# Kernel optimization log

Hardware: AMD Instinct MI355X
Metric: run time of the kernel (lower is better)

The kernel has to match this reference:

```python
import jax, jax.numpy as jnp
import numpy as np

H = 64   # hidden_dim
E = 5    # num_edge_features
F = 6    # num_node_features
B, W, N = 8, 12, 200
LN_EPS = 1e-5


def _lstm_layer(x, Wih, Whh, bih, bhh):
    # x: [BN, W, Fin] -> full output sequence [BN, W, H] (PyTorch gate order i,f,g,o)
    BN = x.shape[0]
    h0 = jnp.zeros((BN, Whh.shape[1]), x.dtype)
    def step(carry, xt):
        h, c = carry
        g = xt @ Wih.T + h @ Whh.T + (bih + bhh)
        i, f, gg, o = jnp.split(g, 4, axis=-1)
        c = jax.nn.sigmoid(f) * c + jax.nn.sigmoid(i) * jnp.tanh(gg)
        h = jax.nn.sigmoid(o) * jnp.tanh(c)
        return (h, c), h
    _, ys = jax.lax.scan(step, (h0, h0), jnp.swapaxes(x, 0, 1))
    return jnp.swapaxes(ys, 0, 1)


def _layernorm(x, g, b):
    mu = jnp.mean(x, axis=-1, keepdims=True)
    var = jnp.mean(jnp.square(x - mu), axis=-1, keepdims=True)
    return (x - mu) * jax.lax.rsqrt(var + LN_EPS) * g + b


def setup_inputs() -> dict:
    key = jax.random.key(0)
    ks = jax.random.split(key, 32)
    s = 0.05
    d = {
        'node_features': jax.random.normal(ks[0], (B, W, N, F), jnp.float32),
        'edge_features': jax.random.normal(ks[1], (B, W, N, N, E), jnp.float32),
        'adjacency': jax.random.uniform(ks[2], (B, N, N), jnp.float32),
        # LSTM layer 0 (input F) and layer 1 (input H)
        'Wih0': jax.random.normal(ks[3], (4 * H, F), jnp.float32) * s,
        'Whh0': jax.random.normal(ks[4], (4 * H, H), jnp.float32) * s,
        'bih0': jax.random.normal(ks[5], (4 * H,), jnp.float32) * s,
        'bhh0': jax.random.normal(ks[6], (4 * H,), jnp.float32) * s,
        'Wih1': jax.random.normal(ks[7], (4 * H, H), jnp.float32) * s,
        'Whh1': jax.random.normal(ks[8], (4 * H, H), jnp.float32) * s,
        'bih1': jax.random.normal(ks[9], (4 * H,), jnp.float32) * s,
        'bhh1': jax.random.normal(ks[10], (4 * H,), jnp.float32) * s,
        # 2 GCN layers: linear, edge projection, layernorm
        'gcn_W': jax.random.normal(ks[11], (2, H, H), jnp.float32) * s,
        'gcn_b': jax.random.normal(ks[12], (2, H), jnp.float32) * s,
        'ep_W': jax.random.normal(ks[13], (2, H, E), jnp.float32) * s,
        'ep_b': jax.random.normal(ks[14], (2, H), jnp.float32) * s,
        'ln_g': jnp.ones((2, H), jnp.float32),
        'ln_b': jnp.zeros((2, H), jnp.float32),
        # edge MLP: (2H+E) -> H -> H//2 -> 1
        'mlp_W1': jax.random.normal(ks[15], (H, 2 * H + E), jnp.float32) * s,
        'mlp_b1': jax.random.normal(ks[16], (H,), jnp.float32) * s,
        'mlp_W2': jax.random.normal(ks[17], (H // 2, H), jnp.float32) * s,
        'mlp_b2': jax.random.normal(ks[18], (H // 2,), jnp.float32) * s,
        'mlp_W3': jax.random.normal(ks[19], (1, H // 2), jnp.float32) * s,
        'mlp_b3': jax.random.normal(ks[20], (1,), jnp.float32) * s,
    }
    return d


def reference(node_features, edge_features, adjacency,
              Wih0, Whh0, bih0, bhh0, Wih1, Whh1, bih1, bhh1,
              gcn_W, gcn_b, ep_W, ep_b, ln_g, ln_b,
              mlp_W1, mlp_b1, mlp_W2, mlp_b2, mlp_W3, mlp_b3):
    Bn, Wn, Nn, _ = node_features.shape
    # [B,W,N,F] -> [B*N, W, F]
    x = jnp.transpose(node_features, (0, 2, 1, 3)).reshape(Bn * Nn, Wn, -1)
    y0 = _lstm_layer(x, Wih0, Whh0, bih0, bhh0)      # dropout between layers: eval mode (identity)
    y1 = _lstm_layer(y0, Wih1, Whh1, bih1, bhh1)
    h = y1[:, -1, :].reshape(Bn, Nn, H)

    edge_last = edge_features[:, -1]                 # [B,N,N,E]
    for i in range(2):
        edge_h = edge_last @ ep_W[i].T + ep_b[i]     # [B,N,N,H]
        messages = jnp.einsum('bij,bijn->bin', adjacency, edge_h)
        updated = h @ gcn_W[i].T + gcn_b[i] + messages
        h = jax.nn.relu(_layernorm(updated, ln_g[i], ln_b[i]))
        # dropout: eval mode (identity)

    h_i = jnp.broadcast_to(h[:, :, None, :], (Bn, Nn, Nn, H))
    h_j = jnp.broadcast_to(h[:, None, :, :], (Bn, Nn, Nn, H))
    edge_input = jnp.concatenate([h_i, h_j, edge_last], axis=-1)  # [B,N,N,2H+E]
    z = jax.nn.relu(edge_input @ mlp_W1.T + mlp_b1)
    z = jax.nn.relu(z @ mlp_W2.T + mlp_b2)
    logits = (z @ mlp_W3.T + mlp_b3)[..., 0]
    return jax.nn.sigmoid(logits)
```

## Files before the change

### kernel.cpp

```cpp
#include <hip/hip_runtime.h>
#include <math.h>


#define Hd   64
#define Ed   5
#define Fd   6
#define Bd   8
#define Wd   12
#define Nd   200
#define NSEQ (Bd*Nd)
#define NG   (4*Hd)
#define NEDGE (Bd*Nd*Nd)
#define LNEPS 1e-5f

__device__ __forceinline__ float sigm(float x) { return 1.0f / (1.0f + __expf(-x)); }
__device__ __forceinline__ float tanh_fast(float x) {
  float ax = fabsf(x);
  float t  = __expf(-2.0f * ax);
  float r  = (1.0f - t) / (1.0f + t);
  return copysignf(r, x);
}

__global__ __launch_bounds__(256) void k_prep(const float* __restrict__ Wih1,
                                              float* __restrict__ Wt1) {
  int k = blockIdx.x;
  int j = threadIdx.x;
  Wt1[k * NG + j] = Wih1[j * Hd + k];
}

__global__ __launch_bounds__(256) void k_lstm0(
    const float* __restrict__ nf,
    const float* __restrict__ Wih0, const float* __restrict__ Whh0,
    const float* __restrict__ bih0, const float* __restrict__ bhh0,
    float* __restrict__ y0)
{
  __shared__ float x_sh[Wd * Fd];
  __shared__ float h_sh[Hd];
  __shared__ float gate_sh[NG];

  const int tid = threadIdx.x;
  const int seq = blockIdx.x;
  const int b = seq / Nd, n = seq % Nd;

  if (tid < Wd * Fd) {
    int t = tid / Fd, f = tid % Fd;
    x_sh[tid] = nf[((b * Wd + t) * Nd + n) * Fd + f];
  }
  if (tid < Hd) h_sh[tid] = 0.f;

  const int j = tid;
  float4 wh[16];
  const float4* wrow = (const float4*)(Whh0 + j * Hd);
  #pragma unroll
  for (int q = 0; q < 16; ++q) wh[q] = wrow[q];
  float wx[Fd];
  #pragma unroll
  for (int f = 0; f < Fd; ++f) wx[f] = Wih0[j * Fd + f];
  const float bias = bih0[j] + bhh0[j];
  const int jt = j >> 6;

  float c = 0.f;
  __syncthreads();

  for (int t = 0; t < Wd; ++t) {
    const float* xp = x_sh + t * Fd;
    float a0 = bias, a1 = 0.f, a2 = 0.f, a3 = 0.f;
    #pragma unroll
    for (int f = 0; f < Fd; ++f) a1 += xp[f] * wx[f];
    const float4* h4 = (const float4*)h_sh;
    #pragma unroll
    for (int q = 0; q < 16; ++q) {
      float4 hv = h4[q];
      float d = hv.x * wh[q].x + hv.y * wh[q].y + hv.z * wh[q].z + hv.w * wh[q].w;
      if ((q & 3) == 0) a0 += d; else if ((q & 3) == 1) a1 += d;
      else if ((q & 3) == 2) a2 += d; else a3 += d;
    }
    float acc = (a0 + a1) + (a2 + a3);
    gate_sh[j] = (jt == 2) ? tanh_fast(acc) : sigm(acc);
    __syncthreads();
    if (tid < Hd) {
      float iv = gate_sh[tid];
      float fv = gate_sh[64 + tid];
      float gv = gate_sh[128 + tid];
      float ov = gate_sh[192 + tid];
      c = fv * c + iv * gv;
      float h = ov * tanh_fast(c);
      h_sh[tid] = h;
      y0[seq * (Wd * Hd) + t * Hd + tid] = h;
    }
    __syncthreads();
  }
}

__global__ __launch_bounds__(256) void k_xproj1(
    const float* __restrict__ y0,
    const float* __restrict__ Wt1,
    const float* __restrict__ bih1, const float* __restrict__ bhh1,
    float* __restrict__ G1)
{
  __shared__ float ysh[64 * 65];
  __shared__ float osh[2 * 64 * 65];

  const int tid  = threadIdx.x;
  const int row0 = blockIdx.x * 64;
  for (int idx = tid; idx < 64 * 64; idx += 256) {
    int r = idx >> 6, k = idx & 63;
    ysh[r * 65 + k] = y0[(row0 + r) * Hd + k];
  }
  __syncthreads();

  const int w = __builtin_amdgcn_readfirstlane(tid >> 6);
  const int r = tid & 63;
  float acc[64];
  #pragma unroll
  for (int c = 0; c < 64; ++c) acc[c] = 0.f;

  const float* wbase = Wt1 + (w << 6);
  #pragma unroll 2
  for (int k = 0; k < 64; ++k) {
    float yv = ysh[r * 65 + k];
    const float* wk = wbase + k * NG;
    #pragma unroll
    for (int c = 0; c < 64; ++c) acc[c] = fmaf(yv, wk[c], acc[c]);
  }
  #pragma unroll
  for (int c = 0; c < 64; ++c) acc[c] += bih1[(w << 6) + c] + bhh1[(w << 6) + c];

  #pragma unroll
  for (int p = 0; p < 2; ++p) {
    __syncthreads();
    if ((w >> 1) == p) {
      float* orow = osh + ((w & 1) * 64 + r) * 65;
      #pragma unroll
      for (int c = 0; c < 64; ++c) orow[c] = acc[c];
    }
    __syncthreads();
    for (int idx = tid; idx < 2 * 64 * 64; idx += 256) {
      int c  = idx & 127;
      int rr = idx >> 7;
      G1[(row0 + rr) * NG + p * 128 + c] =
          osh[((c >> 6) * 64 + rr) * 65 + (c & 63)];
    }
  }
}

__global__ __launch_bounds__(256) void k_lstm1(
    const float* __restrict__ G1,
    const float* __restrict__ Whh1,
    float* __restrict__ hout)
{
  __shared__ float h_sh[Hd];
  __shared__ float gate_sh[NG];

  const int tid = threadIdx.x;
  const int seq = blockIdx.x;
  if (tid < Hd) h_sh[tid] = 0.f;

  const int j = tid;
  float4 wh[16];
  const float4* wrow = (const float4*)(Whh1 + j * Hd);
  #pragma unroll
  for (int q = 0; q < 16; ++q) wh[q] = wrow[q];
  const int jt = j >> 6;
  float c = 0.f;

  float g_cur = G1[(seq * Wd + 0) * NG + j];
  __syncthreads();

  for (int t = 0; t < Wd; ++t) {
    float g_next = (t + 1 < Wd) ? G1[(seq * Wd + t + 1) * NG + j] : 0.f;
    float a0 = g_cur;
    float a1 = 0.f, a2 = 0.f, a3 = 0.f;
    const float4* h4 = (const float4*)h_sh;
    #pragma unroll
    for (int q = 0; q < 16; ++q) {
      float4 hv = h4[q];
      float d = hv.x * wh[q].x + hv.y * wh[q].y + hv.z * wh[q].z + hv.w * wh[q].w;
      if ((q & 3) == 0) a0 += d; else if ((q & 3) == 1) a1 += d;
      else if ((q & 3) == 2) a2 += d; else a3 += d;
    }
    float acc = (a0 + a1) + (a2 + a3);
    gate_sh[j] = (jt == 2) ? tanh_fast(acc) : sigm(acc);
    __syncthreads();
    if (tid < Hd) {
      float iv = gate_sh[tid];
      float fv = gate_sh[64 + tid];
      float gv = gate_sh[128 + tid];
      float ov = gate_sh[192 + tid];
      c = fv * c + iv * gv;
      float h = ov * tanh_fast(c);
      h_sh[tid] = h;
      if (t == Wd - 1) hout[seq * Hd + tid] = h;
    }
    __syncthreads();
    g_cur = g_next;
  }
}

__global__ __launch_bounds__(256) void k_wsum(
    const float* __restrict__ ef, const float* __restrict__ adj,
    float* __restrict__ wsum)
{
  const int row = blockIdx.x;
  const int b = row / Nd, i = row % Nd;
  const int tid = threadIdx.x;
  float p[6] = {0.f, 0.f, 0.f, 0.f, 0.f, 0.f};
  if (tid < Nd) {
    float a = adj[(b * Nd + i) * Nd + tid];
    const float* e = ef + (((b * Wd + (Wd - 1)) * Nd + i) * Nd + tid) * Ed;
    p[5] = a;
    #pragma unroll
    for (int k = 0; k < Ed; ++k) p[k] = a * e[k];
  }
  #pragma unroll
  for (int k = 0; k < 6; ++k) {
    float v = p[k];
    for (int off = 32; off > 0; off >>= 1) v += __shfl_down(v, off);
    p[k] = v;
  }
  __shared__ float red[4][6];
  if ((tid & 63) == 0) {
    #pragma unroll
    for (int k = 0; k < 6; ++k) red[tid >> 6][k] = p[k];
  }
  __syncthreads();
  if (tid < 6)
    wsum[row * 6 + tid] = red[0][tid] + red[1][tid] + red[2][tid] + red[3][tid];
}

__global__ __launch_bounds__(256) void k_gcn(
    const float* __restrict__ hin, const float* __restrict__ wsum,
    const float* __restrict__ gcn_W, const float* __restrict__ gcn_b,
    const float* __restrict__ ep_W,  const float* __restrict__ ep_b,
    const float* __restrict__ ln_g,  const float* __restrict__ ln_b,
    int round, float* __restrict__ hout)
{
  const int row = blockIdx.x * 4 + (threadIdx.x >> 6);
  const int u   = threadIdx.x & 63;
  const float* gw = gcn_W + (round * Hd + u) * Hd;
  const float* ew = ep_W  + (round * Hd + u) * Ed;
  const float* hr = hin + row * Hd;
  const float* wsr = wsum + row * 6;

  float acc = gcn_b[round * Hd + u] + wsr[5] * ep_b[round * Hd + u];
  #pragma unroll
  for (int e = 0; e < Ed; ++e) acc += wsr[e] * ew[e];
  #pragma unroll 8
  for (int k = 0; k < Hd; ++k) acc += hr[k] * gw[k];

  float mu = acc;
  #pragma unroll
  for (int off = 1; off < 64; off <<= 1) mu += __shfl_xor(mu, off);
  mu *= (1.f / 64.f);
  float d = acc - mu;
  float var = d * d;
  #pragma unroll
  for (int off = 1; off < 64; off <<= 1) var += __shfl_xor(var, off);
  var *= (1.f / 64.f);
  float v = d * rsqrtf(var + LNEPS) * ln_g[round * Hd + u] + ln_b[round * Hd + u];
  hout[row * Hd + u] = fmaxf(v, 0.f);
}

__global__ __launch_bounds__(128) void k_uv(
    const float* __restrict__ h, const float* __restrict__ W1,
    const float* __restrict__ b1,
    float* __restrict__ u, float* __restrict__ vt)
{
  const int row = blockIdx.x;
  const int tid = threadIdx.x;
  const float* hr = h + row * Hd;
  if (tid < 64) {
    const float* wr = W1 + tid * 133;
    float acc = b1[tid];
    #pragma unroll 8
    for (int k = 0; k < Hd; ++k) acc += hr[k] * wr[k];
    u[row * Hd + tid] = acc;
  } else {
    const int n = tid - 64;
    const float* wr = W1 + n * 133 + 64;
    float acc = 0.f;
    #pragma unroll 8
    for (int k = 0; k < Hd; ++k) acc += hr[k] * wr[k];
    vt[n * NSEQ + row] = acc;
  }
}

__global__ __launch_bounds__(256) void k_mlp(
    const float* __restrict__ ef,
    const float* __restrict__ u, const float* __restrict__ vt,
    const float* __restrict__ W1,
    const float* __restrict__ W2, const float* __restrict__ b2,
    const float* __restrict__ W3, const float* __restrict__ b3,
    float* __restrict__ out)
{
  const int idx = blockIdx.x * 256 + threadIdx.x;
  const int b   = idx / (Nd * Nd);
  const int rem = idx - b * Nd * Nd;
  const int i   = rem / Nd;
  const int jj  = rem - i * Nd;

  const float* e = ef + (((b * Wd + (Wd - 1)) * Nd + i) * Nd + jj) * Ed;
  float e5[Ed];
  #pragma unroll
  for (int q = 0; q < Ed; ++q) e5[q] = e[q];

  const float* ur = u + (b * Nd + i) * Hd;
  const int vcol = b * Nd + jj;

  float z1[64];
  #pragma unroll
  for (int k = 0; k < 64; ++k) {
    float acc = ur[k] + vt[k * NSEQ + vcol];
    const float* w1c = W1 + k * 133 + 128;
    #pragma unroll
    for (int q = 0; q < Ed; ++q) acc += e5[q] * w1c[q];
    z1[k] = fmaxf(acc, 0.f);
  }

  float logit = b3[0];
  #pragma unroll 4
  for (int o = 0; o < 32; ++o) {
    float a0 = b2[o], a1 = 0.f, a2 = 0.f, a3 = 0.f;
    const float* w2 = W2 + o * 64;
    #pragma unroll
    for (int k = 0; k < 64; k += 4) {
      a0 += w2[k]     * z1[k];
      a1 += w2[k + 1] * z1[k + 1];
      a2 += w2[k + 2] * z1[k + 2];
      a3 += w2[k + 3] * z1[k + 3];
    }
    float z2 = fmaxf((a0 + a1) + (a2 + a3), 0.f);
    logit += W3[o] * z2;
  }
  out[idx] = 1.f / (1.f + __expf(-logit));
}

extern "C" void kernel_launch(void* const* d_in, const int* in_sizes, int n_in,
                              void* d_out, int out_size, void* d_ws, size_t ws_size,
                              hipStream_t stream) {
  (void)in_sizes; (void)n_in; (void)out_size; (void)ws_size;
  const float* nf   = (const float*)d_in[0];
  const float* ef   = (const float*)d_in[1];
  const float* adj  = (const float*)d_in[2];
  const float* Wih0 = (const float*)d_in[3];
  const float* Whh0 = (const float*)d_in[4];
  const float* bih0 = (const float*)d_in[5];
  const float* bhh0 = (const float*)d_in[6];
  const float* Wih1 = (const float*)d_in[7];
  const float* Whh1 = (const float*)d_in[8];
  const float* bih1 = (const float*)d_in[9];
  const float* bhh1 = (const float*)d_in[10];
  const float* gcnW = (const float*)d_in[11];
  const float* gcnB = (const float*)d_in[12];
  const float* epW  = (const float*)d_in[13];
  const float* epB  = (const float*)d_in[14];
  const float* lnG  = (const float*)d_in[15];
  const float* lnB  = (const float*)d_in[16];
  const float* W1   = (const float*)d_in[17];
  const float* b1   = (const float*)d_in[18];
  const float* W2   = (const float*)d_in[19];
  const float* b2   = (const float*)d_in[20];
  const float* W3   = (const float*)d_in[21];
  const float* b3   = (const float*)d_in[22];
  float* out = (float*)d_out;

  float* ws  = (float*)d_ws;
  float* y0  = ws;
  float* G1  = y0  + 1228800;
  float* Wt1 = G1  + 4915200;
  float* h0  = Wt1 + 16384;
  float* wsm = h0  + 102400;
  float* hA  = wsm + 9600;
  float* hB  = hA  + 102400;
  float* uu  = hB  + 102400;
  float* vt  = uu  + 102400;

  k_prep  <<<64,   256, 0, stream>>>(Wih1, Wt1);
  k_lstm0 <<<NSEQ, 256, 0, stream>>>(nf, Wih0, Whh0, bih0, bhh0, y0);
  k_xproj1<<<300,  256, 0, stream>>>(y0, Wt1, bih1, bhh1, G1);
  k_lstm1 <<<NSEQ, 256, 0, stream>>>(G1, Whh1, h0);
  k_wsum  <<<1600, 256, 0, stream>>>(ef, adj, wsm);
  k_gcn   <<<400,  256, 0, stream>>>(h0, wsm, gcnW, gcnB, epW, epB, lnG, lnB, 0, hA);
  k_gcn   <<<400,  256, 0, stream>>>(hA, wsm, gcnW, gcnB, epW, epB, lnG, lnB, 1, hB);
  k_uv    <<<1600, 128, 0, stream>>>(hB, W1, b1, uu, vt);
  k_mlp   <<<1250, 256, 0, stream>>>(ef, uu, vt, W1, W2, b2, W3, b3, out);
}
```

Measured before the change: 277.2 us.

## Compute all LSTM gates per thread in one wave and fuse node-stage kernels

Both LSTM kernels now run one 64-thread wavefront per sequence. Each thread keeps all four gate rows of the recurrent weights in registers and computes i, f, g, o and the cell update itself. This removes the shared gate buffer and one block barrier per timestep, at the cost of about four times the serial FMA work per thread and much higher register pressure. The adjacency/edge weighted-sum, both GCN rounds and the u/v projection are merged into one per-row kernel. That removes three launches and the intermediate global buffers, though most threads in that fused kernel sit idle during the GCN and projection phases.

```diff
diff --git a/kernel.cpp b/kernel.cpp
--- a/kernel.cpp
+++ b/kernel.cpp
@@ -28,7 +28,7 @@
   Wt1[k * NG + j] = Wih1[j * Hd + k];
 }
 
-__global__ __launch_bounds__(256) void k_lstm0(
+__global__ __launch_bounds__(64, 1) void k_lstm0(
     const float* __restrict__ nf,
     const float* __restrict__ Wih0, const float* __restrict__ Whh0,
     const float* __restrict__ bih0, const float* __restrict__ bhh0,
@@ -36,59 +36,66 @@
 {
   __shared__ float x_sh[Wd * Fd];
   __shared__ float h_sh[Hd];
-  __shared__ float gate_sh[NG];
-
-  const int tid = threadIdx.x;
+
+  const int u   = threadIdx.x;
   const int seq = blockIdx.x;
   const int b = seq / Nd, n = seq % Nd;
 
-  if (tid < Wd * Fd) {
-    int t = tid / Fd, f = tid % Fd;
-    x_sh[tid] = nf[((b * Wd + t) * Nd + n) * Fd + f];
-  }
-  if (tid < Hd) h_sh[tid] = 0.f;
-
-  const int j = tid;
-  float4 wh[16];
-  const float4* wrow = (const float4*)(Whh0 + j * Hd);
-  #pragma unroll
-  for (int q = 0; q < 16; ++q) wh[q] = wrow[q];
-  float wx[Fd];
-  #pragma unroll
-  for (int f = 0; f < Fd; ++f) wx[f] = Wih0[j * Fd + f];
-  const float bias = bih0[j] + bhh0[j];
-  const int jt = j >> 6;
+  for (int idx = u; idx < Wd * Fd; idx += 64) {
+    int t = idx / Fd, f = idx % Fd;
+    x_sh[idx] = nf[((b * Wd + t) * Nd + n) * Fd + f];
+  }
+  h_sh[u] = 0.f;
+
+  float4 wh[4][16];
+  #pragma unroll
+  for (int g = 0; g < 4; ++g) {
+    const float4* wrow = (const float4*)(Whh0 + (g * 64 + u) * Hd);
+    #pragma unroll
+    for (int q = 0; q < 16; ++q) wh[g][q] = wrow[q];
+  }
+  float wx[4][Fd];
+  #pragma unroll
+  for (int g = 0; g < 4; ++g)
+    #pragma unroll
+    for (int f = 0; f < Fd; ++f) wx[g][f] = Wih0[(g * 64 + u) * Fd + f];
+  float bias[4];
+  #pragma unroll
+  for (int g = 0; g < 4; ++g) bias[g] = bih0[g * 64 + u] + bhh0[g * 64 + u];
 
   float c = 0.f;
   __syncthreads();
 
   for (int t = 0; t < Wd; ++t) {
-    const float* xp = x_sh + t * Fd;
-    float a0 = bias, a1 = 0.f, a2 = 0.f, a3 = 0.f;
-    #pragma unroll
-    for (int f = 0; f < Fd; ++f) a1 += xp[f] * wx[f];
+    float xv[Fd];
+    #pragma unroll
+    for (int f = 0; f < Fd; ++f) xv[f] = x_sh[t * Fd + f];
+    float4 hv[16];
     const float4* h4 = (const float4*)h_sh;
     #pragma unroll
-    for (int q = 0; q < 16; ++q) {
-      float4 hv = h4[q];
-      float d = hv.x * wh[q].x + hv.y * wh[q].y + hv.z * wh[q].z + hv.w * wh[q].w;
-      if ((q & 3) == 0) a0 += d; else if ((q & 3) == 1) a1 += d;
-      else if ((q & 3) == 2) a2 += d; else a3 += d;
-    }
-    float acc = (a0 + a1) + (a2 + a3);
-    gate_sh[j] = (jt == 2) ? tanh_fast(acc) : sigm(acc);
-    __syncthreads();
-    if (tid < Hd) {
-      float iv = gate_sh[tid];
-      float fv = gate_sh[64 + tid];
-      float gv = gate_sh[128 + tid];
-      float ov = gate_sh[192 + tid];
-      c = fv * c + iv * gv;
-      float h = ov * tanh_fast(c);
-      h_sh[tid] = h;
-      y0[seq * (Wd * Hd) + t * Hd + tid] = h;
-    }
-    __syncthreads();
+    for (int q = 0; q < 16; ++q) hv[q] = h4[q];
+
+    float g4[4];
+    #pragma unroll
+    for (int g = 0; g < 4; ++g) {
+      float a0 = bias[g], a1 = 0.f, a2 = 0.f, a3 = 0.f;
+      #pragma unroll
+      for (int f = 0; f < Fd; ++f) a1 += xv[f] * wx[g][f];
+      #pragma unroll
+      for (int q = 0; q < 16; ++q) {
+        float d = hv[q].x * wh[g][q].x + hv[q].y * wh[g][q].y +
+                  hv[q].z * wh[g][q].z + hv[q].w * wh[g][q].w;
+        if ((q & 3) == 0) a0 += d; else if ((q & 3) == 1) a1 += d;
+        else if ((q & 3) == 2) a2 += d; else a3 += d;
+      }
+      float acc = (a0 + a1) + (a2 + a3);
+      g4[g] = (g == 2) ? tanh_fast(acc) : sigm(acc);
+    }
+    c = g4[1] * c + g4[0] * g4[2];
+    float h = g4[3] * tanh_fast(c);
+    h_sh[u] = h;
+    __syncthreads();
+    y0[seq * (Wd * Hd) + t * Hd + u] = h;
   }
 }
 
@@ -144,66 +151,84 @@
   }
 }
 
-__global__ __launch_bounds__(256) void k_lstm1(
+__global__ __launch_bounds__(64, 1) void k_lstm1(
     const float* __restrict__ G1,
     const float* __restrict__ Whh1,
     float* __restrict__ hout)
 {
   __shared__ float h_sh[Hd];
-  __shared__ float gate_sh[NG];
-
-  const int tid = threadIdx.x;
+
+  const int u   = threadIdx.x;
   const int seq = blockIdx.x;
-  if (tid < Hd) h_sh[tid] = 0.f;
-
-  const int j = tid;
-  float4 wh[16];
-  const float4* wrow = (const float4*)(Whh1 + j * Hd);
-  #pragma unroll
-  for (int q = 0; q < 16; ++q) wh[q] = wrow[q];
-  const int jt = j >> 6;
+  h_sh[u] = 0.f;
+
+  float4 wh[4][16];
+  #pragma unroll
+  for (int g = 0; g < 4; ++g) {
+    const float4* wrow = (const float4*)(Whh1 + (g * 64 + u) * Hd);
+    #pragma unroll
+    for (int q = 0; q < 16; ++q) wh[g][q] = wrow[q];
+  }
   float c = 0.f;
 
-  float g_cur = G1[(seq * Wd + 0) * NG + j];
+  float gc[4];
+  #pragma unroll
+  for (int g = 0; g < 4; ++g) gc[g] = G1[(seq * Wd + 0) * NG + g * 64 + u];
   __syncthreads();
 
   for (int t = 0; t < Wd; ++t) {
-    float g_next = (t + 1 < Wd) ? G1[(seq * Wd + t + 1) * NG + j] : 0.f;
-    float a0 = g_cur;
-    float a1 = 0.f, a2 = 0.f, a3 = 0.f;
+    float gn[4];
+    #pragma unroll
+    for (int g = 0; g < 4; ++g)
+      gn[g] = (t + 1 < Wd) ? G1[(seq * Wd + t + 1) * NG + g * 64 + u] : 0.f;
+
+    float4 hv[16];
     const float4* h4 = (const float4*)h_sh;
     #pragma unroll
-    for (int q = 0; q < 16; ++q) {
-      float4 hv = h4[q];
-      float d = hv.x * wh[q].x + hv.y * wh[q].y + hv.z * wh[q].z + hv.w * wh[q].w;
-      if ((q & 3) == 0) a0 += d; else if ((q & 3) == 1) a1 += d;
-      else if ((q & 3) == 2) a2 += d; else a3 += d;
-    }
-    float acc = (a0 + a1) + (a2 + a3);
-    gate_sh[j] = (jt == 2) ? tanh_fast(acc) : sigm(acc);
-    __syncthreads();
-    if (tid < Hd) {
-      float iv = gate_sh[tid];
-      float fv = gate_sh[64 + tid];
-      float gv = gate_sh[128 + tid];
-      float ov = gate_sh[192 + tid];
-      c = fv * c + iv * gv;
-      float h = ov * tanh_fast(c);
-      h_sh[tid] = h;
-      if (t == Wd - 1) hout[seq * Hd + tid] = h;
-    }
-    __syncthreads();
-    g_cur = g_next;
-  }
-}
-
-__global__ __launch_bounds__(256) void k_wsum(
-    const float* __restrict__ ef, const float* __restrict__ adj,
-    float* __restrict__ wsum)
-{
+    for (int q = 0; q < 16; ++q) hv[q] = h4[q];
+
+    float g4[4];
+    #pragma unroll
+    for (int g = 0; g < 4; ++g) {
+      float a0 = gc[g];
+      float a1 = 0.f, a2 = 0.f, a3 = 0.f;
+      #pragma unroll
+      for (int q = 0; q < 16; ++q) {
+        float d = hv[q].x * wh[g][q].x + hv[q].y * wh[g][q].y +
+                  hv[q].z * wh[g][q].z + hv[q].w * wh[g][q].w;
+        if ((q & 3) == 0) a0 += d; else if ((q & 3) == 1) a1 += d;
+        else if ((q & 3) == 2) a2 += d; else a3 += d;
+      }
+      float acc = (a0 + a1) + (a2 + a3);
+      g4[g] = (g == 2) ? tanh_fast(acc) : sigm(acc);
+    }
+    c = g4[1] * c + g4[0] * g4[2];
+    float h = g4[3] * tanh_fast(c);
+    h_sh[u] = h;
+    __syncthreads();
+    if (t == Wd - 1) hout[seq * Hd + u] = h;
+    #pragma unroll
+    for (int g = 0; g < 4; ++g) gc[g] = gn[g];
+  }
+}
+
+__global__ __launch_bounds__(256) void k_node(
+    const float* __restrict__ ef,    const float* __restrict__ adj,
+    const float* __restrict__ h0,
+    const float* __restrict__ gcn_W, const float* __restrict__ gcn_b,
+    const float* __restrict__ ep_W,  const float* __restrict__ ep_b,
+    const float* __restrict__ ln_g,  const float* __restrict__ ln_b,
+    const float* __restrict__ W1,    const float* __restrict__ b1,
+    float* __restrict__ uu, float* __restrict__ vt)
+{
+  __shared__ float red[4][6];
+  __shared__ float w6[6];
+  __shared__ float hcur[Hd];
+
   const int row = blockIdx.x;
   const int b = row / Nd, i = row % Nd;
   const int tid = threadIdx.x;
+
   float p[6] = {0.f, 0.f, 0.f, 0.f, 0.f, 0.f};
   if (tid < Nd) {
     float a = adj[(b * Nd + i) * Nd + tid];
@@ -218,69 +243,58 @@
     for (int off = 32; off > 0; off >>= 1) v += __shfl_down(v, off);
     p[k] = v;
   }
-  __shared__ float red[4][6];
   if ((tid & 63) == 0) {
     #pragma unroll
     for (int k = 0; k < 6; ++k) red[tid >> 6][k] = p[k];
   }
   __syncthreads();
   if (tid < 6)
-    wsum[row * 6 + tid] = red[0][tid] + red[1][tid] + red[2][tid] + red[3][tid];
-}
-
-__global__ __launch_bounds__(256) void k_gcn(
-    const float* __restrict__ hin, const float* __restrict__ wsum,
-    const float* __restrict__ gcn_W, const float* __restrict__ gcn_b,
-    const float* __restrict__ ep_W,  const float* __restrict__ ep_b,
-    const float* __restrict__ ln_g,  const float* __restrict__ ln_b,
-    int round, float* __restrict__ hout)
-{
-  const int row = blockIdx.x * 4 + (threadIdx.x >> 6);
-  const int u   = threadIdx.x & 63;
-  const float* gw = gcn_W + (round * Hd + u) * Hd;
-  const float* ew = ep_W  + (round * Hd + u) * Ed;
-  const float* hr = hin + row * Hd;
-  const float* wsr = wsum + row * 6;
-
-  float acc = gcn_b[round * Hd + u] + wsr[5] * ep_b[round * Hd + u];
-  #pragma unroll
-  for (int e = 0; e < Ed; ++e) acc += wsr[e] * ew[e];
-  #pragma unroll 8
-  for (int k = 0; k < Hd; ++k) acc += hr[k] * gw[k];
-
-  float mu = acc;
-  #pragma unroll
-  for (int off = 1; off < 64; off <<= 1) mu += __shfl_xor(mu, off);
-  mu *= (1.f / 64.f);
-  float d = acc - mu;
-  float var = d * d;
-  #pragma unroll
-  for (int off = 1; off < 64; off <<= 1) var += __shfl_xor(var, off);
-  var *= (1.f / 64.f);
-  float v = d * rsqrtf(var + LNEPS) * ln_g[round * Hd + u] + ln_b[round * Hd + u];
-  hout[row * Hd + u] = fmaxf(v, 0.f);
-}
-
-__global__ __launch_bounds__(128) void k_uv(
-    const float* __restrict__ h, const float* __restrict__ W1,
-    const float* __restrict__ b1,
-    float* __restrict__ u, float* __restrict__ vt)
-{
-  const int row = blockIdx.x;
-  const int tid = threadIdx.x;
-  const float* hr = h + row * Hd;
+    w6[tid] = red[0][tid] + red[1][tid] + red[2][tid] + red[3][tid];
+  if (tid < Hd) hcur[tid] = h0[row * Hd + tid];
+  __syncthreads();
+
+  const int u = tid & 63;
+  #pragma unroll
+  for (int round = 0; round < 2; ++round) {
+    float hnew = 0.f;
+    if (tid < 64) {
+      const float* gw = gcn_W + (round * Hd + u) * Hd;
+      const float* ew = ep_W  + (round * Hd + u) * Ed;
+      float acc = gcn_b[round * Hd + u] + w6[5] * ep_b[round * Hd + u];
+      #pragma unroll
+      for (int e = 0; e < Ed; ++e) acc += w6[e] * ew[e];
+      #pragma unroll 8
+      for (int k = 0; k < Hd; ++k) acc += hcur[k] * gw[k];
+
+      float mu = acc;
+      #pragma unroll
+      for (int off = 1; off < 64; off <<= 1) mu += __shfl_xor(mu, off);
+      mu *= (1.f / 64.f);
+      float d = acc - mu;
+      float var = d * d;
+      #pragma unroll
+      for (int off = 1; off < 64; off <<= 1) var += __shfl_xor(var, off);
+      var *= (1.f / 64.f);
+      float v = d * rsqrtf(var + LNEPS) * ln_g[round * Hd + u] + ln_b[round * Hd + u];
+      hnew = fmaxf(v, 0.f);
+    }
+    __syncthreads();
+    if (tid < 64) hcur[tid] = hnew;
+    __syncthreads();
+  }
+
   if (tid < 64) {
     const float* wr = W1 + tid * 133;
     float acc = b1[tid];
     #pragma unroll 8
-    for (int k = 0; k < Hd; ++k) acc += hr[k] * wr[k];
-    u[row * Hd + tid] = acc;
-  } else {
+    for (int k = 0; k < Hd; ++k) acc += hcur[k] * wr[k];
+    uu[row * Hd + tid] = acc;
+  } else if (tid < 128) {
     const int n = tid - 64;
     const float* wr = W1 + n * 133 + 64;
     float acc = 0.f;
     #pragma unroll 8
-    for (int k = 0; k < Hd; ++k) acc += hr[k] * wr[k];
+    for (int k = 0; k < Hd; ++k) acc += hcur[k] * wr[k];
     vt[n * NSEQ + row] = acc;
   }
 }
@@ -369,19 +383,14 @@
   float* G1  = y0  + 1228800;
   float* Wt1 = G1  + 4915200;
   float* h0  = Wt1 + 16384;
-  float* wsm = h0  + 102400;
-  float* hA  = wsm + 9600;
-  float* hB  = hA  + 102400;
-  float* uu  = hB  + 102400;
+  float* uu  = h0  + 102400;
   float* vt  = uu  + 102400;
 
   k_prep  <<<64,   256, 0, stream>>>(Wih1, Wt1);
-  k_lstm0 <<<NSEQ, 256, 0, stream>>>(nf, Wih0, Whh0, bih0, bhh0, y0);
+  k_lstm0 <<<NSEQ, 64,  0, stream>>>(nf, Wih0, Whh0, bih0, bhh0, y0);
   k_xproj1<<<300,  256, 0, stream>>>(y0, Wt1, bih1, bhh1, G1);
-  k_lstm1 <<<NSEQ, 256, 0, stream>>>(G1, Whh1, h0);
-  k_wsum  <<<1600, 256, 0, stream>>>(ef, adj, wsm);
-  k_gcn   <<<400,  256, 0, stream>>>(h0, wsm, gcnW, gcnB, epW, epB, lnG, lnB, 0, hA);
-  k_gcn   <<<400,  256, 0, stream>>>(hA, wsm, gcnW, gcnB, epW, epB, lnG, lnB, 1, hB);
-  k_uv    <<<1600, 128, 0, stream>>>(hB, W1, b1, uu, vt);
+  k_lstm1 <<<NSEQ, 64,  0, stream>>>(G1, Whh1, h0);
+  k_node  <<<1600, 256, 0, stream>>>(ef, adj, h0, gcnW, gcnB, epW, epB,
+                                     lnG, lnB, W1, b1, uu, vt);
   k_mlp   <<<1250, 256, 0, stream>>>(ef, uu, vt, W1, W2, b2, W3, b3, out);
 }
```

New measurement: 309.7 us. +11.7%, slower.

## Double-buffer LSTM gates to drop a barrier and fuse node-stage kernels

Applied to the files above, without the earlier changes.

Both LSTM recurrence kernels now double-buffer the gate array and let every wave redundantly compute the cell/hidden update. This removes the second __syncthreads per timestep. Weight registers are pinned and an occupancy hint is added. The edge-weighted sum, both GCN rounds and the MLP first-layer node projections are fused into one kernel, eliminating three launches and intermediate global buffers. The cost is redundant cell math in all waves and low thread utilization in the fused node kernel.

```diff
diff --git a/kernel.cpp b/kernel.cpp
--- a/kernel.cpp
+++ b/kernel.cpp
@@ -13,6 +13,8 @@
 #define NEDGE (Bd*Nd*Nd)
 #define LNEPS 1e-5f
 
+#define PIN4(v) asm volatile("" : "+v"((v).x), "+v"((v).y), "+v"((v).z), "+v"((v).w))
+
 __device__ __forceinline__ float sigm(float x) { return 1.0f / (1.0f + __expf(-x)); }
 __device__ __forceinline__ float tanh_fast(float x) {
   float ax = fabsf(x);
@@ -28,7 +30,7 @@
   Wt1[k * NG + j] = Wih1[j * Hd + k];
 }
 
-__global__ __launch_bounds__(256) void k_lstm0(
+__global__ __launch_bounds__(256, 3) void k_lstm0(
     const float* __restrict__ nf,
     const float* __restrict__ Wih0, const float* __restrict__ Whh0,
     const float* __restrict__ bih0, const float* __restrict__ bhh0,
@@ -36,23 +38,24 @@
 {
   __shared__ float x_sh[Wd * Fd];
   __shared__ float h_sh[Hd];
-  __shared__ float gate_sh[NG];
+  __shared__ float gate_sh[2][NG];
 
   const int tid = threadIdx.x;
   const int seq = blockIdx.x;
   const int b = seq / Nd, n = seq % Nd;
+  const int u = tid & 63;
 
   if (tid < Wd * Fd) {
     int t = tid / Fd, f = tid % Fd;
     x_sh[tid] = nf[((b * Wd + t) * Nd + n) * Fd + f];
   }
-  if (tid < Hd) h_sh[tid] = 0.f;
+  h_sh[u] = 0.f;
 
   const int j = tid;
   float4 wh[16];
   const float4* wrow = (const float4*)(Whh0 + j * Hd);
   #pragma unroll
-  for (int q = 0; q < 16; ++q) wh[q] = wrow[q];
+  for (int q = 0; q < 16; ++q) { wh[q] = wrow[q]; PIN4(wh[q]); }
   float wx[Fd];
   #pragma unroll
   for (int f = 0; f < Fd; ++f) wx[f] = Wih0[j * Fd + f];
@@ -76,19 +79,17 @@
       else if ((q & 3) == 2) a2 += d; else a3 += d;
     }
     float acc = (a0 + a1) + (a2 + a3);
-    gate_sh[j] = (jt == 2) ? tanh_fast(acc) : sigm(acc);
-    __syncthreads();
-    if (tid < Hd) {
-      float iv = gate_sh[tid];
-      float fv = gate_sh[64 + tid];
-      float gv = gate_sh[128 + tid];
-      float ov = gate_sh[192 + tid];
-      c = fv * c + iv * gv;
-      float h = ov * tanh_fast(c);
-      h_sh[tid] = h;
-      y0[seq * (Wd * Hd) + t * Hd + tid] = h;
-    }
-    __syncthreads();
+    gate_sh[t & 1][j] = (jt == 2) ? tanh_fast(acc) : sigm(acc);
+    __syncthreads();
+    const float* gb = gate_sh[t & 1];
+    float iv = gb[u];
+    float fv = gb[64 + u];
+    float gv = gb[128 + u];
+    float ov = gb[192 + u];
+    c = fv * c + iv * gv;
+    float h = ov * tanh_fast(c);
+    h_sh[u] = h;
+    if (tid < Hd) y0[seq * (Wd * Hd) + t * Hd + u] = h;
   }
 }
 
@@ -144,23 +145,24 @@
   }
 }
 
-__global__ __launch_bounds__(256) void k_lstm1(
+__global__ __launch_bounds__(256, 3) void k_lstm1(
     const float* __restrict__ G1,
     const float* __restrict__ Whh1,
     float* __restrict__ hout)
 {
   __shared__ float h_sh[Hd];
-  __shared__ float gate_sh[NG];
+  __shared__ float gate_sh[2][NG];
 
   const int tid = threadIdx.x;
   const int seq = blockIdx.x;
-  if (tid < Hd) h_sh[tid] = 0.f;
+  const int u = tid & 63;
+  h_sh[u] = 0.f;
 
   const int j = tid;
   float4 wh[16];
   const float4* wrow = (const float4*)(Whh1 + j * Hd);
   #pragma unroll
-  for (int q = 0; q < 16; ++q) wh[q] = wrow[q];
+  for (int q = 0; q < 16; ++q) { wh[q] = wrow[q]; PIN4(wh[q]); }
   const int jt = j >> 6;
   float c = 0.f;
 
@@ -180,30 +182,38 @@
       else if ((q & 3) == 2) a2 += d; else a3 += d;
     }
     float acc = (a0 + a1) + (a2 + a3);
-    gate_sh[j] = (jt == 2) ? tanh_fast(acc) : sigm(acc);
-    __syncthreads();
-    if (tid < Hd) {
-      float iv = gate_sh[tid];
-      float fv = gate_sh[64 + tid];
-      float gv = gate_sh[128 + tid];
-      float ov = gate_sh[192 + tid];
-      c = fv * c + iv * gv;
-      float h = ov * tanh_fast(c);
-      h_sh[tid] = h;
-      if (t == Wd - 1) hout[seq * Hd + tid] = h;
-    }
-    __syncthreads();
+    gate_sh[t & 1][j] = (jt == 2) ? tanh_fast(acc) : sigm(acc);
+    __syncthreads();
+    const float* gb = gate_sh[t & 1];
+    float iv = gb[u];
+    float fv = gb[64 + u];
+    float gv = gb[128 + u];
+    float ov = gb[192 + u];
+    c = fv * c + iv * gv;
+    float h = ov * tanh_fast(c);
+    h_sh[u] = h;
+    if (t == Wd - 1 && tid < Hd) hout[seq * Hd + u] = h;
     g_cur = g_next;
   }
 }
 
-__global__ __launch_bounds__(256) void k_wsum(
-    const float* __restrict__ ef, const float* __restrict__ adj,
-    float* __restrict__ wsum)
-{
+__global__ __launch_bounds__(256) void k_node(
+    const float* __restrict__ ef,    const float* __restrict__ adj,
+    const float* __restrict__ h0,
+    const float* __restrict__ gcn_W, const float* __restrict__ gcn_b,
+    const float* __restrict__ ep_W,  const float* __restrict__ ep_b,
+    const float* __restrict__ ln_g,  const float* __restrict__ ln_b,
+    const float* __restrict__ W1,    const float* __restrict__ b1,
+    float* __restrict__ uu, float* __restrict__ vt)
+{
+  __shared__ float red[4][6];
+  __shared__ float w6[6];
+  __shared__ float hcur[Hd];
+
   const int row = blockIdx.x;
   const int b = row / Nd, i = row % Nd;
   const int tid = threadIdx.x;
+
   float p[6] = {0.f, 0.f, 0.f, 0.f, 0.f, 0.f};
   if (tid < Nd) {
     float a = adj[(b * Nd + i) * Nd + tid];
@@ -218,69 +228,58 @@
     for (int off = 32; off > 0; off >>= 1) v += __shfl_down(v, off);
     p[k] = v;
   }
-  __shared__ float red[4][6];
   if ((tid & 63) == 0) {
     #pragma unroll
     for (int k = 0; k < 6; ++k) red[tid >> 6][k] = p[k];
   }
   __syncthreads();
   if (tid < 6)
-    wsum[row * 6 + tid] = red[0][tid] + red[1][tid] + red[2][tid] + red[3][tid];
-}
-
-__global__ __launch_bounds__(256) void k_gcn(
-    const float* __restrict__ hin, const float* __restrict__ wsum,
-    const float* __restrict__ gcn_W, const float* __restrict__ gcn_b,
-    const float* __restrict__ ep_W,  const float* __restrict__ ep_b,
-    const float* __restrict__ ln_g,  const float* __restrict__ ln_b,
-    int round, float* __restrict__ hout)
-{
-  const int row = blockIdx.x * 4 + (threadIdx.x >> 6);
-  const int u   = threadIdx.x & 63;
-  const float* gw = gcn_W + (round * Hd + u) * Hd;
-  const float* ew = ep_W  + (round * Hd + u) * Ed;
-  const float* hr = hin + row * Hd;
-  const float* wsr = wsum + row * 6;
-
-  float acc = gcn_b[round * Hd + u] + wsr[5] * ep_b[round * Hd + u];
-  #pragma unroll
-  for (int e = 0; e < Ed; ++e) acc += wsr[e] * ew[e];
-  #pragma unroll 8
-  for (int k = 0; k < Hd; ++k) acc += hr[k] * gw[k];
-
-  float mu = acc;
-  #pragma unroll
-  for (int off = 1; off < 64; off <<= 1) mu += __shfl_xor(mu, off);
-  mu *= (1.f / 64.f);
-  float d = acc - mu;
-  float var = d * d;
-  #pragma unroll
-  for (int off = 1; off < 64; off <<= 1) var += __shfl_xor(var, off);
-  var *= (1.f / 64.f);
-  float v = d * rsqrtf(var + LNEPS) * ln_g[round * Hd + u] + ln_b[round * Hd + u];
-  hout[row * Hd + u] = fmaxf(v, 0.f);
-}
-
-__global__ __launch_bounds__(128) void k_uv(
-    const float* __restrict__ h, const float* __restrict__ W1,
-    const float* __restrict__ b1,
-    float* __restrict__ u, float* __restrict__ vt)
-{
-  const int row = blockIdx.x;
-  const int tid = threadIdx.x;
-  const float* hr = h + row * Hd;
+    w6[tid] = red[0][tid] + red[1][tid] + red[2][tid] + red[3][tid];
+  if (tid < Hd) hcur[tid] = h0[row * Hd + tid];
+  __syncthreads();
+
+  const int u = tid & 63;
+  #pragma unroll
+  for (int round = 0; round < 2; ++round) {
+    float hnew = 0.f;
+    if (tid < 64) {
+      const float* gw = gcn_W + (round * Hd + u) * Hd;
+      const float* ew = ep_W  + (round * Hd + u) * Ed;
+      float acc = gcn_b[round * Hd + u] + w6[5] * ep_b[round * Hd + u];
+      #pragma unroll
+      for (int e = 0; e < Ed; ++e) acc += w6[e] * ew[e];
+      #pragma unroll 8
+      for (int k = 0; k < Hd; ++k) acc += hcur[k] * gw[k];
+
+      float mu = acc;
+      #pragma unroll
+      for (int off = 1; off < 64; off <<= 1) mu += __shfl_xor(mu, off);
+      mu *= (1.f / 64.f);
+      float d = acc - mu;
+      float var = d * d;
+      #pragma unroll
+      for (int off = 1; off < 64; off <<= 1) var += __shfl_xor(var, off);
+      var *= (1.f / 64.f);
+      float v = d * rsqrtf(var + LNEPS) * ln_g[round * Hd + u] + ln_b[round * Hd + u];
+      hnew = fmaxf(v, 0.f);
+    }
+    __syncthreads();
+    if (tid < 64) hcur[tid] = hnew;
+    __syncthreads();
+  }
+
   if (tid < 64) {
     const float* wr = W1 + tid * 133;
     float acc = b1[tid];
     #pragma unroll 8
-    for (int k = 0; k < Hd; ++k) acc += hr[k] * wr[k];
-    u[row * Hd + tid] = acc;
-  } else {
+    for (int k = 0; k < Hd; ++k) acc += hcur[k] * wr[k];
+    uu[row * Hd + tid] = acc;
+  } else if (tid < 128) {
     const int n = tid - 64;
     const float* wr = W1 + n * 133 + 64;
     float acc = 0.f;
     #pragma unroll 8
-    for (int k = 0; k < Hd; ++k) acc += hr[k] * wr[k];
+    for (int k = 0; k < Hd; ++k) acc += hcur[k] * wr[k];
     vt[n * NSEQ + row] = acc;
   }
 }
@@ -369,19 +368,14 @@
   float* G1  = y0  + 1228800;
   float* Wt1 = G1  + 4915200;
   float* h0  = Wt1 + 16384;
-  float* wsm = h0  + 102400;
-  float* hA  = wsm + 9600;
-  float* hB  = hA  + 102400;
-  float* uu  = hB  + 102400;
+  float* uu  = h0  + 102400;
   float* vt  = uu  + 102400;
 
   k_prep  <<<64,   256, 0, stream>>>(Wih1, Wt1);
   k_lstm0 <<<NSEQ, 256, 0, stream>>>(nf, Wih0, Whh0, bih0, bhh0, y0);
   k_xproj1<<<300,  256, 0, stream>>>(y0, Wt1, bih1, bhh1, G1);
   k_lstm1 <<<NSEQ, 256, 0, stream>>>(G1, Whh1, h0);
-  k_wsum  <<<1600, 256, 0, stream>>>(ef, adj, wsm);
-  k_gcn   <<<400,  256, 0, stream>>>(h0, wsm, gcnW, gcnB, epW, epB, lnG, lnB, 0, hA);
-  k_gcn   <<<400,  256, 0, stream>>>(hA, wsm, gcnW, gcnB, epW, epB, lnG, lnB, 1, hB);
-  k_uv    <<<1600, 128, 0, stream>>>(hB, W1, b1, uu, vt);
+  k_node  <<<1600, 256, 0, stream>>>(ef, adj, h0, gcnW, gcnB, epW, epB,
+                                     lnG, lnB, W1, b1, uu, vt);
   k_mlp   <<<1250, 256, 0, stream>>>(ef, uu, vt, W1, W2, b2, W3, b3, out);
 }
```

Measured after the change: 282.5 us. No clear change (+1.9%).
